# Kernel tuning notes

Hardware: AMD Instinct MI355X
Metric: run time of the kernel (lower is better)

## Reference

```python
import jax, jax.numpy as jnp
import numpy as np

B, T, TKV, D, H = 4, 2048, 512, 1024, 16
HD = D // H  # 64
HIDDEN = ((int(D * 4 * 2 / 3) + 7) // 8) * 8  # 2736
EPS = 1e-6


def setup_inputs() -> dict:
    key = jax.random.key(0)
    ks = jax.random.split(key, 16)
    x = jax.random.normal(ks[0], (B, T, D), jnp.float32)
    memory = jax.random.normal(ks[1], (B, TKV, D), jnp.float32)
    # RoPE frequencies: (T, HD//2, 2) = (cos, sin)
    inv_freq = 1.0 / (10000.0 ** (jnp.arange(0, HD, 2, dtype=jnp.float32) / HD))
    angles = jnp.arange(T, dtype=jnp.float32)[:, None] * inv_freq[None, :]
    freqs_cis = jnp.stack([jnp.cos(angles), jnp.sin(angles)], axis=-1)
    # causal mask (T, T): 0 on/below diag, -inf above
    causal_mask = jnp.where(jnp.tril(jnp.ones((T, T), bool)), 0.0, -jnp.inf).astype(jnp.float32)
    s = 0.02
    w = lambda k, i, o: jax.random.normal(k, (i, o), jnp.float32) * s  # stored as (in, out)
    return {
        'x': x, 'memory': memory, 'freqs_cis': freqs_cis, 'causal_mask': causal_mask,
        'sa_wq': w(ks[2], D, D), 'sa_wk': w(ks[3], D, D), 'sa_wv': w(ks[4], D, D), 'sa_wo': w(ks[5], D, D),
        'ca_wq': w(ks[6], D, D), 'ca_wk': w(ks[7], D, D), 'ca_wv': w(ks[8], D, D), 'ca_wo': w(ks[9], D, D),
        'w1': w(ks[10], D, HIDDEN), 'w3': w(ks[11], D, HIDDEN), 'w2': w(ks[12], HIDDEN, D),
        'g_sa': jnp.ones((D,), jnp.float32), 'g_ca': jnp.ones((D,), jnp.float32), 'g_ffn': jnp.ones((D,), jnp.float32),
    }


def rmsnorm(x, g):
    return x * jax.lax.rsqrt(jnp.mean(x * x, axis=-1, keepdims=True) + EPS) * g


def apply_rope(t, f):
    # t: (B, H, T, HD); f: (T, HD//2, 2)
    tr = t.reshape(*t.shape[:-1], HD // 2, 2)
    a, b = tr[..., 0], tr[..., 1]
    cos, sin = f[None, None, :, :, 0], f[None, None, :, :, 1]
    out = jnp.stack([a * cos - b * sin, a * sin + b * cos], axis=-1)
    return out.reshape(t.shape)


def heads(x, w):
    # (B, S, D) @ (D, D) -> (B, H, S, HD)
    b, s, _ = x.shape
    return (x @ w).reshape(b, s, H, HD).transpose(0, 2, 1, 3)


def attention(xq, kv, wq, wk, wv, wo, freqs=None, mask=None):
    q, k, v = heads(xq, wq), heads(kv, wk), heads(kv, wv)
    if freqs is not None:
        q, k = apply_rope(q, freqs), apply_rope(k, freqs)
    attn = jnp.einsum('bhqd,bhkd->bhqk', q, k) * (HD ** -0.5)
    if mask is not None:
        attn = attn + mask
    attn = jax.nn.softmax(attn, axis=-1)
    out = jnp.einsum('bhqk,bhkd->bhqd', attn, v)
    out = out.transpose(0, 2, 1, 3).reshape(xq.shape[0], xq.shape[1], D)
    return out @ wo


def reference(x, memory, freqs_cis, causal_mask,
              sa_wq, sa_wk, sa_wv, sa_wo,
              ca_wq, ca_wk, ca_wv, ca_wo,
              w1, w2, w3, g_sa, g_ca, g_ffn):
    x = rmsnorm(x + attention(x, x, sa_wq, sa_wk, sa_wv, sa_wo, freqs=freqs_cis, mask=causal_mask), g_sa)
    x = rmsnorm(x + attention(x, memory, ca_wq, ca_wk, ca_wv, ca_wo), g_ca)
    ffn = (jax.nn.silu(x @ w1) * (x @ w3)) @ w2
    x = rmsnorm(x + ffn, g_ffn)
    return x
```

## Files before the change

### kernel.cpp

```cpp
#include <hip/hip_runtime.h>
#include <hip/hip_bf16.h>

typedef __attribute__((ext_vector_type(8))) short s16x8;
typedef __attribute__((ext_vector_type(4))) float f32x4;
typedef __attribute__((ext_vector_type(16))) float f32x16;
typedef unsigned short u16;
typedef unsigned int u32;
typedef unsigned long long u64;

#define MFMA(a,b,c) __builtin_amdgcn_mfma_f32_16x16x32_bf16(a,b,c,0,0,0)
#define MFMA32(a,b,c) __builtin_amdgcn_mfma_f32_32x32x16_bf16(a,b,c,0,0,0)

constexpr int B_ = 4, T_ = 2048, TKV_ = 512, D_ = 1024, H_ = 16, HD_ = 64;
constexpr int HID_ = 2736, HIDP_ = 2816;

__device__ __forceinline__ float bf2f(u16 x) {
    union { float f; u32 u; } c; c.u = ((u32)x) << 16; return c.f;
}
__device__ __forceinline__ u16 f2bf(float f) {
    union { float f; u32 u; } c; c.f = f;
    u32 r = c.u + 0x7fffu + ((c.u >> 16) & 1u);
    return (u16)(r >> 16);
}

__device__ __forceinline__ void gload16(const void* g, void* l) {
    __builtin_amdgcn_global_load_lds(
        (const __attribute__((address_space(1))) u32*)g,
        (__attribute__((address_space(3))) u32*)l, 16, 0, 0);
}

__global__ __launch_bounds__(256) void wt_cast(const float* __restrict__ W, u16* __restrict__ WT,
                                               int K, int N, int Kp, int Np) {
    __shared__ float t[32][33];
    int tid = threadIdx.x;
    int tx = tid & 31, ty = tid >> 5;
    int n0 = blockIdx.x * 32, k0 = blockIdx.y * 32;
#pragma unroll
    for (int i = 0; i < 4; ++i) {
        int kk = k0 + ty + i * 8, nn = n0 + tx;
        t[ty + i * 8][tx] = (kk < K && nn < N) ? W[(size_t)kk * N + nn] : 0.f;
    }
    __syncthreads();
#pragma unroll
    for (int i = 0; i < 4; ++i) {
        int nn = n0 + ty + i * 8, kk = k0 + tx;
        WT[(size_t)nn * Kp + kk] = f2bf(t[tx][ty + i * 8]);
    }
}

__global__ __launch_bounds__(256) void cast_bf16(const float* __restrict__ in, u16* __restrict__ out, int n4) {
    int i = blockIdx.x * 256 + threadIdx.x;
    if (i >= n4) return;
    float4 v = ((const float4*)in)[i];
    u64 pk = (u64)f2bf(v.x) | ((u64)f2bf(v.y) << 16) | ((u64)f2bf(v.z) << 32) | ((u64)f2bf(v.w) << 48);
    ((u64*)out)[i] = pk;
}

__device__ __forceinline__ void gemm_store(void* C, const u16* mul, size_t idx, float v, int mode) {
    if (mode == 0) {
        ((float*)C)[idx] = v;
    } else if (mode == 1) {
        ((u16*)C)[idx] = f2bf(v);
    } else if (mode == 2) {
        float sg = 1.f / (1.f + __expf(-v));
        ((u16*)C)[idx] = f2bf(v * sg);
    } else if (mode == 3) {
        float h = bf2f(mul[idx]);
        ((u16*)C)[idx] = f2bf(v * h);
    } else {
        ((u16*)C)[idx] = f2bf(v * 0.125f);
    }
}


__global__ __launch_bounds__(256) void gemm_bf16(const u16* __restrict__ A, const u16* __restrict__ Bt,
                                                 void* __restrict__ C, const u16* __restrict__ mul,
                                                 int M, int N, int K, int mode, int nwg) {
    __shared__ __align__(16) u16 As[128 * 64];
    __shared__ __align__(16) u16 Bs[128 * 64];
    const int tid = threadIdx.x;
    const int lane = tid & 63, wid = tid >> 6;
    const int wr = wid >> 1, wc = wid & 1;
    const int li = lane & 15, g = lane >> 4;

    int bid = (int)blockIdx.x;
    bid = (bid & 7) * (nwg >> 3) + (bid >> 3);

    const int tn = N >> 7;
    const int m0 = (bid / tn) * 128, n0 = (bid % tn) * 128;

    const int rowst = tid >> 3;
    const int colb = (((tid & 7) ^ ((tid >> 3) & 7)) * 16);
    const char* ga = (const char*)A + ((size_t)(m0 + rowst) * K) * 2 + colb;
    const char* gb = (const char*)Bt + ((size_t)(n0 + rowst) * K) * 2 + colb;
    const size_t rstride = (size_t)32 * K * 2;

    f32x4 acc[4][4] = {};
    const int nt = K >> 6;

    for (int t = 0; t < nt; ++t) {
#pragma unroll
        for (int i = 0; i < 4; ++i) {
            gload16(ga + (size_t)t * 128 + i * rstride, (char*)As + i * 4096 + wid * 1024);
            gload16(gb + (size_t)t * 128 + i * rstride, (char*)Bs + i * 4096 + wid * 1024);
        }
        __syncthreads();
#pragma unroll
        for (int kk = 0; kk < 2; ++kk) {
            s16x8 aF[4], bF[4];
            const int sl = ((kk << 2) | g) ^ (li & 7);
#pragma unroll
            for (int m = 0; m < 4; ++m) aF[m] = *(const s16x8*)&As[(wr * 64 + m * 16 + li) * 64 + sl * 8];
#pragma unroll
            for (int n = 0; n < 4; ++n) bF[n] = *(const s16x8*)&Bs[(wc * 64 + n * 16 + li) * 64 + sl * 8];
#pragma unroll
            for (int m = 0; m < 4; ++m)
#pragma unroll
                for (int n = 0; n < 4; ++n)
                    acc[m][n] = MFMA(aF[m], bF[n], acc[m][n]);
        }
        __syncthreads();
    }

#pragma unroll
    for (int m = 0; m < 4; ++m)
#pragma unroll
        for (int n = 0; n < 4; ++n)
#pragma unroll
            for (int r = 0; r < 4; ++r) {
                size_t row = m0 + wr * 64 + m * 16 + g * 4 + r;
                size_t col = n0 + wc * 64 + n * 16 + li;
                gemm_store(C, mul, row * N + col, acc[m][n][r], mode);
            }
}

__global__ __launch_bounds__(256) void gemm_w13(const u16* __restrict__ A, const u16* __restrict__ B1t,
                                                const u16* __restrict__ B3t, u16* __restrict__ Hout,
                                                int M, int N, int K, int nwg) {
    __shared__ __align__(16) u16 As[128 * 64];
    __shared__ __align__(16) u16 B1s[128 * 64];
    __shared__ __align__(16) u16 B3s[128 * 64];
    const int tid = threadIdx.x;
    const int lane = tid & 63, wid = tid >> 6;
    const int wr = wid >> 1, wc = wid & 1;
    const int li = lane & 15, g = lane >> 4;

    int bid = (int)blockIdx.x;
    bid = (bid & 7) * (nwg >> 3) + (bid >> 3);

    const int tn = N >> 7;
    const int m0 = (bid / tn) * 128, n0 = (bid % tn) * 128;

    const int rowst = tid >> 3;
    const int colb = (((tid & 7) ^ ((tid >> 3) & 7)) * 16);
    const char* ga = (const char*)A + ((size_t)(m0 + rowst) * K) * 2 + colb;
    const char* gb1 = (const char*)B1t + ((size_t)(n0 + rowst) * K) * 2 + colb;
    const char* gb3 = (const char*)B3t + ((size_t)(n0 + rowst) * K) * 2 + colb;
    const size_t rstride = (size_t)32 * K * 2;

    f32x4 acc1[4][4] = {}, acc3[4][4] = {};
    const int nt = K >> 6;

    for (int t = 0; t < nt; ++t) {
#pragma unroll
        for (int i = 0; i < 4; ++i) {
            gload16(ga + (size_t)t * 128 + i * rstride, (char*)As + i * 4096 + wid * 1024);
            gload16(gb1 + (size_t)t * 128 + i * rstride, (char*)B1s + i * 4096 + wid * 1024);
            gload16(gb3 + (size_t)t * 128 + i * rstride, (char*)B3s + i * 4096 + wid * 1024);
        }
        __syncthreads();
#pragma unroll
        for (int kk = 0; kk < 2; ++kk) {
            const int sl = ((kk << 2) | g) ^ (li & 7);
            s16x8 aF[4];
#pragma unroll
            for (int m = 0; m < 4; ++m) aF[m] = *(const s16x8*)&As[(wr * 64 + m * 16 + li) * 64 + sl * 8];
            {
                s16x8 bF[4];
#pragma unroll
                for (int n = 0; n < 4; ++n) bF[n] = *(const s16x8*)&B1s[(wc * 64 + n * 16 + li) * 64 + sl * 8];
#pragma unroll
                for (int m = 0; m < 4; ++m)
#pragma unroll
                    for (int n = 0; n < 4; ++n)
                        acc1[m][n] = MFMA(aF[m], bF[n], acc1[m][n]);
            }
            {
                s16x8 bF[4];
#pragma unroll
                for (int n = 0; n < 4; ++n) bF[n] = *(const s16x8*)&B3s[(wc * 64 + n * 16 + li) * 64 + sl * 8];
#pragma unroll
                for (int m = 0; m < 4; ++m)
#pragma unroll
                    for (int n = 0; n < 4; ++n)
                        acc3[m][n] = MFMA(aF[m], bF[n], acc3[m][n]);
            }
        }
        __syncthreads();
    }

#pragma unroll
    for (int m = 0; m < 4; ++m)
#pragma unroll
        for (int n = 0; n < 4; ++n)
#pragma unroll
            for (int r = 0; r < 4; ++r) {
                size_t row = m0 + wr * 64 + m * 16 + g * 4 + r;
                size_t col = n0 + wc * 64 + n * 16 + li;
                float h1 = acc1[m][n][r];
                float h3 = acc3[m][n][r];
                float sg = 1.f / (1.f + __expf(-h1));
                Hout[row * N + col] = f2bf(h1 * sg * h3);
            }
}

__global__ __launch_bounds__(256) void rope_qk(u16* __restrict__ q, u16* __restrict__ k,
                                               const float* __restrict__ fr, int S) {
    size_t idx = (size_t)blockIdx.x * 256 + threadIdx.x;
    int i = (int)(idx & 31);
    int h = (int)((idx >> 5) & 15);
    size_t bt = idx >> 9;
    int t = (int)(bt & (T_ - 1));
    float2 cs = ((const float2*)fr)[t * 32 + i];
    size_t off = bt * (size_t)S + h * 64 + 2 * i;
    {
        u32* p = (u32*)(q + off);
        u32 w = *p;
        float a = bf2f((u16)(w & 0xffff)), b = bf2f((u16)(w >> 16));
        *p = (u32)f2bf((a * cs.x - b * cs.y) * 0.125f) | ((u32)f2bf((a * cs.y + b * cs.x) * 0.125f) << 16);
    }
    {
        u32* p = (u32*)(k + off);
        u32 w = *p;
        float a = bf2f((u16)(w & 0xffff)), b = bf2f((u16)(w >> 16));
        *p = (u32)f2bf(a * cs.x - b * cs.y) | ((u32)f2bf(a * cs.y + b * cs.x) << 16);
    }
}

__global__ __launch_bounds__(256) void vtrans(const u16* __restrict__ v, u16* __restrict__ vT,
                                              int Tk, int S) {
    __shared__ u16 tile[32][34];
    int bh = blockIdx.x;
    int t0 = blockIdx.y * 32, d0 = blockIdx.z * 32;
    int b = bh >> 4, h = bh & 15;
    int tid = threadIdx.x;
    int tx = tid & 31, ty = tid >> 5;
#pragma unroll
    for (int i = 0; i < 4; ++i)
        tile[ty + i * 8][tx] = v[((size_t)b * Tk + t0 + ty + i * 8) * S + h * 64 + d0 + tx];
    __syncthreads();
#pragma unroll
    for (int i = 0; i < 4; ++i)
        vT[((size_t)bh * 64 + d0 + ty + i * 8) * Tk + t0 + tx] = tile[tx][ty + i * 8];
}

__device__ __forceinline__ void attn32(const u16* __restrict__ qh, const u16* __restrict__ kh,
                                       const u16* __restrict__ vh, u16* __restrict__ oh,
                                       int q0, int nkb, int Tk, int causal, int lq, int hi,
                                       int QS, int KS) {
    const u16* qb = qh + (size_t)(q0 + lq) * QS;
    s16x8 qf[4];
#pragma unroll
    for (int c = 0; c < 4; ++c) qf[c] = *(const s16x8*)&qb[c * 16 + hi * 8];

    f32x16 o0 = {}, o1 = {};
    float mr = -1e30f, lr = 0.f;

    for (int kb = 0; kb < nkb; ++kb) {
        const int ks = kb * 32;
        f32x16 s = {};
        const u16* kp = kh + (size_t)(ks + lq) * KS + hi * 8;
#pragma unroll
        for (int c = 0; c < 4; ++c) {
            s16x8 kf = *(const s16x8*)&kp[c * 16];
            s = MFMA32(kf, qf[c], s);
        }
        if (causal && kb == nkb - 1) {
#pragma unroll
            for (int r = 0; r < 16; ++r) {
                int kl = (r & 3) + 8 * (r >> 2) + 4 * hi;
                if (kl > lq) s[r] = -1e30f;
            }
        }
        float bm = fmaxf(fmaxf(fmaxf(s[0], s[1]), fmaxf(s[2], s[3])),
                         fmaxf(fmaxf(s[4], s[5]), fmaxf(s[6], s[7])));
        float bm2 = fmaxf(fmaxf(fmaxf(s[8], s[9]), fmaxf(s[10], s[11])),
                          fmaxf(fmaxf(s[12], s[13]), fmaxf(s[14], s[15])));
        bm = fmaxf(bm, bm2);
        bm = fmaxf(bm, __shfl_xor(bm, 32));
        float mn = fmaxf(mr, bm);
        float sc = __expf(mr - mn);
        mr = mn;
        float p[16];
        float rs = 0.f;
#pragma unroll
        for (int r = 0; r < 16; ++r) { p[r] = __expf(s[r] - mn); rs += p[r]; }
        rs += __shfl_xor(rs, 32);
        lr = lr * sc + rs;
#pragma unroll
        for (int r = 0; r < 16; ++r) { o0[r] *= sc; o1[r] *= sc; }

        u32 pk[8];
#pragma unroll
        for (int i = 0; i < 8; ++i)
            pk[i] = (u32)f2bf(p[2 * i]) | ((u32)f2bf(p[2 * i + 1]) << 16);
        u32 e1 = __shfl_xor(hi ? pk[0] : pk[2], 32);
        u32 e2 = __shfl_xor(hi ? pk[1] : pk[3], 32);
        u32 e3 = __shfl_xor(hi ? pk[4] : pk[6], 32);
        u32 e4 = __shfl_xor(hi ? pk[5] : pk[7], 32);
        union { s16x8 v; u32 w[4]; } pf0, pf1;
        pf0.w[0] = hi ? e1 : pk[0];
        pf0.w[1] = hi ? e2 : pk[1];
        pf0.w[2] = hi ? pk[2] : e1;
        pf0.w[3] = hi ? pk[3] : e2;
        pf1.w[0] = hi ? e3 : pk[4];
        pf1.w[1] = hi ? e4 : pk[5];
        pf1.w[2] = hi ? pk[6] : e3;
        pf1.w[3] = hi ? pk[7] : e4;

        const u16* v0 = vh + (size_t)lq * Tk + ks + hi * 8;
        const u16* v1 = vh + (size_t)(32 + lq) * Tk + ks + hi * 8;
        o0 = MFMA32(*(const s16x8*)&v0[0],  pf0.v, o0);
        o0 = MFMA32(*(const s16x8*)&v0[16], pf1.v, o0);
        o1 = MFMA32(*(const s16x8*)&v1[0],  pf0.v, o1);
        o1 = MFMA32(*(const s16x8*)&v1[16], pf1.v, o1);
    }

    float inv = 1.f / lr;
    u16* ob = oh + (size_t)(q0 + lq) * D_;
#pragma unroll
    for (int r = 0; r < 16; ++r) {
        int hd = (r & 3) + 8 * (r >> 2) + 4 * hi;
        ob[hd] = f2bf(o0[r] * inv);
        ob[hd + 32] = f2bf(o1[r] * inv);
    }
}

__global__ __launch_bounds__(256) void attn_causal32(const u16* __restrict__ q, const u16* __restrict__ k,
                                                     const u16* __restrict__ vT, u16* __restrict__ o,
                                                     int Tq, int Tk, int QS, int KS) {
    const int lane = threadIdx.x & 63, wid = threadIdx.x >> 6;
    const int lq = lane & 31, hi = lane >> 5;
    const int ntile = Tq / 32;
    const int ppb = (ntile / 2) / 4;
    const int bh = blockIdx.x / ppb;
    const int p = (blockIdx.x % ppb) * 4 + wid;
    const int b = bh >> 4, h = bh & 15;

    const u16* qh = q + ((size_t)b * Tq) * QS + h * 64;
    const u16* kh = k + ((size_t)b * Tk) * KS + h * 64;
    const u16* vh = vT + ((size_t)bh * 64) * Tk;
    u16* oh = o + ((size_t)b * Tq) * D_ + h * 64;

    const int tA = p, tB = ntile - 1 - p;
    attn32(qh, kh, vh, oh, tA * 32, tA + 1, Tk, 1, lq, hi, QS, KS);
    attn32(qh, kh, vh, oh, tB * 32, tB + 1, Tk, 1, lq, hi, QS, KS);
}

__global__ __launch_bounds__(256) void attn_plain32(const u16* __restrict__ q, const u16* __restrict__ k,
                                                    const u16* __restrict__ vT, u16* __restrict__ o,
                                                    int Tq, int Tk, int QS, int KS) {
    const int lane = threadIdx.x & 63, wid = threadIdx.x >> 6;
    const int lq = lane & 31, hi = lane >> 5;
    const int tpb = (Tq / 32) / 4;
    const int bh = blockIdx.x / tpb;
    const int qt = (blockIdx.x % tpb) * 4 + wid;
    const int b = bh >> 4, h = bh & 15;

    const u16* qh = q + ((size_t)b * Tq) * QS + h * 64;
    const u16* kh = k + ((size_t)b * Tk) * KS + h * 64;
    const u16* vh = vT + ((size_t)bh * 64) * Tk;
    u16* oh = o + ((size_t)b * Tq) * D_ + h * 64;

    attn32(qh, kh, vh, oh, qt * 32, Tk / 32, Tk, 0, lq, hi, QS, KS);
}

__global__ __launch_bounds__(256) void addnorm(const float* __restrict__ xa, const u16* __restrict__ xb,
                                               const float* __restrict__ gg, float* __restrict__ fo,
                                               u16* __restrict__ bo) {
    int row = blockIdx.x * 4 + (threadIdx.x >> 6);
    int lane = threadIdx.x & 63;
    const float4* pa = (const float4*)(xa + (size_t)row * D_);
    const u64* pb = (const u64*)(xb + (size_t)row * D_);
    float4 v[4];
    float ss = 0.f;
#pragma unroll
    for (int j = 0; j < 4; ++j) {
        float4 a = pa[lane + 64 * j];
        u64 bw = pb[lane + 64 * j];
        v[j].x = a.x + bf2f((u16)(bw));
        v[j].y = a.y + bf2f((u16)(bw >> 16));
        v[j].z = a.z + bf2f((u16)(bw >> 32));
        v[j].w = a.w + bf2f((u16)(bw >> 48));
        ss += v[j].x * v[j].x + v[j].y * v[j].y + v[j].z * v[j].z + v[j].w * v[j].w;
    }
    ss += __shfl_xor(ss, 1);
    ss += __shfl_xor(ss, 2);
    ss += __shfl_xor(ss, 4);
    ss += __shfl_xor(ss, 8);
    ss += __shfl_xor(ss, 16);
    ss += __shfl_xor(ss, 32);
    float s = rsqrtf(ss * (1.0f / D_) + 1e-6f);
#pragma unroll
    for (int j = 0; j < 4; ++j) {
        float4 gv = ((const float4*)gg)[lane + 64 * j];
        float yx = v[j].x * s * gv.x, yy = v[j].y * s * gv.y;
        float yz = v[j].z * s * gv.z, yw = v[j].w * s * gv.w;
        if (fo) {
            float4 o4; o4.x = yx; o4.y = yy; o4.z = yz; o4.w = yw;
            ((float4*)(fo + (size_t)row * D_))[lane + 64 * j] = o4;
        }
        if (bo) {
            u64 pk = (u64)f2bf(yx) | ((u64)f2bf(yy) << 16) | ((u64)f2bf(yz) << 32) | ((u64)f2bf(yw) << 48);
            ((u64*)(bo + (size_t)row * D_))[lane + 64 * j] = pk;
        }
    }
}

extern "C" void kernel_launch(void* const* d_in, const int* in_sizes, int n_in,
                              void* d_out, int out_size, void* d_ws, size_t ws_size,
                              hipStream_t stream) {
    const float* x    = (const float*)d_in[0];
    const float* mem  = (const float*)d_in[1];
    const float* fr   = (const float*)d_in[2];
    const float* wsaq = (const float*)d_in[4];
    const float* wsak = (const float*)d_in[5];
    const float* wsav = (const float*)d_in[6];
    const float* wsao = (const float*)d_in[7];
    const float* wcaq = (const float*)d_in[8];
    const float* wcak = (const float*)d_in[9];
    const float* wcav = (const float*)d_in[10];
    const float* wcao = (const float*)d_in[11];
    const float* w1   = (const float*)d_in[12];
    const float* w3   = (const float*)d_in[13];
    const float* w2   = (const float*)d_in[14];
    const float* g_sa = (const float*)d_in[15];
    const float* g_ca = (const float*)d_in[16];
    const float* g_ff = (const float*)d_in[17];
    float* outF = (float*)d_out;

    char* p = (char*)d_ws;
    auto alloc = [&](size_t bytes) { char* r = p; p += (bytes + 255) & ~(size_t)255; return r; };
    const size_t DD2 = (size_t)1024 * 1024 * 2;
    u16* wqkvT = (u16*)alloc(3 * DD2);
    u16* saoT  = (u16*)alloc(DD2);
    u16* caqT  = (u16*)alloc(DD2);
    u16* wkvT  = (u16*)alloc(2 * DD2);
    u16* caoT  = (u16*)alloc(DD2);
    u16* w1T   = (u16*)alloc((size_t)HIDP_ * 1024 * 2);
    u16* w3T   = (u16*)alloc((size_t)HIDP_ * 1024 * 2);
    u16* w2T   = (u16*)alloc((size_t)1024 * HIDP_ * 2);
    u16* Ab    = (u16*)alloc((size_t)8192 * 1024 * 2);
    u16* memb  = (u16*)alloc((size_t)2048 * 1024 * 2);
    char* qkvRaw = alloc((size_t)8192 * 3072 * 2);
    u16* qkvb = (u16*)qkvRaw;
    u16* kvb  = (u16*)qkvRaw;
    u16* caqb = (u16*)(qkvRaw + (size_t)25165824);
    u16* vtb  = (u16*)alloc((size_t)8192 * 1024 * 2);
    u16* ob   = (u16*)alloc((size_t)8192 * 1024 * 2);
    u16* Pb   = (u16*)alloc((size_t)8192 * 1024 * 2);
    float* Rf = (float*)alloc((size_t)8192 * 1024 * 4);
    u16* Hb   = (u16*)alloc((size_t)8192 * HIDP_ * 2);

    dim3 blk(256);

    wt_cast<<<dim3(32, 32), blk, 0, stream>>>(wsaq, wqkvT,               1024, 1024, 1024, 1024);
    wt_cast<<<dim3(32, 32), blk, 0, stream>>>(wsak, wqkvT + 1024 * 1024, 1024, 1024, 1024, 1024);
    wt_cast<<<dim3(32, 32), blk, 0, stream>>>(wsav, wqkvT + 2048 * 1024, 1024, 1024, 1024, 1024);
    wt_cast<<<dim3(32, 32), blk, 0, stream>>>(wsao, saoT, 1024, 1024, 1024, 1024);
    wt_cast<<<dim3(32, 32), blk, 0, stream>>>(wcaq, caqT, 1024, 1024, 1024, 1024);
    wt_cast<<<dim3(32, 32), blk, 0, stream>>>(wcak, wkvT,               1024, 1024, 1024, 1024);
    wt_cast<<<dim3(32, 32), blk, 0, stream>>>(wcav, wkvT + 1024 * 1024, 1024, 1024, 1024, 1024);
    wt_cast<<<dim3(32, 32), blk, 0, stream>>>(wcao, caoT, 1024, 1024, 1024, 1024);
    wt_cast<<<dim3(88, 32), blk, 0, stream>>>(w1, w1T, 1024, HID_, 1024, HIDP_);
    wt_cast<<<dim3(88, 32), blk, 0, stream>>>(w3, w3T, 1024, HID_, 1024, HIDP_);
    wt_cast<<<dim3(32, 88), blk, 0, stream>>>(w2, w2T, HID_, 1024, HIDP_, 1024);

    cast_bf16<<<8192, blk, 0, stream>>>(x, Ab, 2097152);
    cast_bf16<<<2048, blk, 0, stream>>>(mem, memb, 524288);

    gemm_bf16<<<1536, blk, 0, stream>>>(Ab, wqkvT, qkvb, nullptr, 8192, 3072, 1024, 1, 1536);
    rope_qk<<<16384, blk, 0, stream>>>(qkvb, qkvb + 1024, fr, 3072);
    vtrans<<<dim3(64, 64, 2), blk, 0, stream>>>(qkvb + 2048, vtb, 2048, 3072);
    attn_causal32<<<512, blk, 0, stream>>>(qkvb, qkvb + 1024, vtb, ob, 2048, 2048, 3072, 3072);
    gemm_bf16<<<512, blk, 0, stream>>>(ob, saoT, Pb, nullptr, 8192, 1024, 1024, 1, 512);
    addnorm<<<2048, blk, 0, stream>>>(x, Pb, g_sa, Rf, Ab);

    gemm_bf16<<<512, blk, 0, stream>>>(Ab, caqT, caqb, nullptr, 8192, 1024, 1024, 4, 512);
    gemm_bf16<<<256, blk, 0, stream>>>(memb, wkvT, kvb, nullptr, 2048, 2048, 1024, 1, 256);
    vtrans<<<dim3(64, 16, 2), blk, 0, stream>>>(kvb + 1024, vtb, 512, 2048);
    attn_plain32<<<1024, blk, 0, stream>>>(caqb, kvb, vtb, ob, 2048, 512, 1024, 2048);
    gemm_bf16<<<512, blk, 0, stream>>>(ob, caoT, Pb, nullptr, 8192, 1024, 1024, 1, 512);
    addnorm<<<2048, blk, 0, stream>>>(Rf, Pb, g_ca, Rf, Ab);

    gemm_w13<<<1408, blk, 0, stream>>>(Ab, w1T, w3T, Hb, 8192, HIDP_, 1024, 1408);
    gemm_bf16<<<512, blk, 0, stream>>>(Hb, w2T, Pb, nullptr, 8192, 1024, HIDP_, 1, 512);
    addnorm<<<2048, blk, 0, stream>>>(Rf, Pb, g_ff, outF, nullptr);
}
```

Before: 801.9 us.

## Fuse paired causal query tiles into one KV loop sharing K/V loads

The causal attention kernel used to process its two balanced query tiles (p and ntile-1-p) in sequence, loading K and V twice. Both tiles now run in a single loop over KV blocks. Each K and V fragment is loaded once and feeds both tiles' MFMAs, and tile A's work is predicated off once its diagonal is passed. Global/L2 traffic for K/V and loop overhead drop, at the cost of roughly doubling the accumulator registers, which may reduce occupancy or cause spills.

```diff
diff --git a/kernel.cpp b/kernel.cpp
--- a/kernel.cpp
+++ b/kernel.cpp
@@ -254,6 +254,58 @@
         vT[((size_t)bh * 64 + d0 + ty + i * 8) * Tk + t0 + tx] = tile[tx][ty + i * 8];
 }
 
+__device__ __forceinline__ void sm_pack(const f32x16& s, int hi, float& mr, float& lr,
+                                        f32x16& o0, f32x16& o1, s16x8& pf0v, s16x8& pf1v) {
+    float bm = fmaxf(fmaxf(fmaxf(s[0], s[1]), fmaxf(s[2], s[3])),
+                     fmaxf(fmaxf(s[4], s[5]), fmaxf(s[6], s[7])));
+    float bm2 = fmaxf(fmaxf(fmaxf(s[8], s[9]), fmaxf(s[10], s[11])),
+                      fmaxf(fmaxf(s[12], s[13]), fmaxf(s[14], s[15])));
+    bm = fmaxf(bm, bm2);
+    bm = fmaxf(bm, __shfl_xor(bm, 32));
+    float mn = fmaxf(mr, bm);
+    float sc = __expf(mr - mn);
+    mr = mn;
+    float p[16];
+    float rs = 0.f;
+#pragma unroll
+    for (int r = 0; r < 16; ++r) { p[r] = __expf(s[r] - mn); rs += p[r]; }
+    rs += __shfl_xor(rs, 32);
+    lr = lr * sc + rs;
+#pragma unroll
+    for (int r = 0; r < 16; ++r) { o0[r] *= sc; o1[r] *= sc; }
+
+    u32 pk[8];
+#pragma unroll
+    for (int i = 0; i < 8; ++i)
+        pk[i] = (u32)f2bf(p[2 * i]) | ((u32)f2bf(p[2 * i + 1]) << 16);
+    u32 e1 = __shfl_xor(hi ? pk[0] : pk[2], 32);
+    u32 e2 = __shfl_xor(hi ? pk[1] : pk[3], 32);
+    u32 e3 = __shfl_xor(hi ? pk[4] : pk[6], 32);
+    u32 e4 = __shfl_xor(hi ? pk[5] : pk[7], 32);
+    union { s16x8 v; u32 w[4]; } pf0, pf1;
+    pf0.w[0] = hi ? e1 : pk[0];
+    pf0.w[1] = hi ? e2 : pk[1];
+    pf0.w[2] = hi ? pk[2] : e1;
+    pf0.w[3] = hi ? pk[3] : e2;
+    pf1.w[0] = hi ? e3 : pk[4];
+    pf1.w[1] = hi ? e4 : pk[5];
+    pf1.w[2] = hi ? pk[6] : e3;
+    pf1.w[3] = hi ? pk[7] : e4;
+    pf0v = pf0.v;
+    pf1v = pf1.v;
+}
+
+__device__ __forceinline__ void attn_out(u16* ob, const f32x16& o0, const f32x16& o1,
+                                         float lr, int hi) {
+    float inv = 1.f / lr;
+#pragma unroll
+    for (int r = 0; r < 16; ++r) {
+        int hd = (r & 3) + 8 * (r >> 2) + 4 * hi;
+        ob[hd] = f2bf(o0[r] * inv);
+        ob[hd + 32] = f2bf(o1[r] * inv);
+    }
+}
+
 __device__ __forceinline__ void attn32(const u16* __restrict__ qh, const u16* __restrict__ kh,
                                        const u16* __restrict__ vh, u16* __restrict__ oh,
                                        int q0, int nkb, int Tk, int causal, int lq, int hi,
@@ -282,63 +334,22 @@
                 if (kl > lq) s[r] = -1e30f;
             }
         }
-        float bm = fmaxf(fmaxf(fmaxf(s[0], s[1]), fmaxf(s[2], s[3])),
-                         fmaxf(fmaxf(s[4], s[5]), fmaxf(s[6], s[7])));
-        float bm2 = fmaxf(fmaxf(fmaxf(s[8], s[9]), fmaxf(s[10], s[11])),
-                          fmaxf(fmaxf(s[12], s[13]), fmaxf(s[14], s[15])));
-        bm = fmaxf(bm, bm2);
-        bm = fmaxf(bm, __shfl_xor(bm, 32));
-        float mn = fmaxf(mr, bm);
-        float sc = __expf(mr - mn);
-        mr = mn;
-        float p[16];
-        float rs = 0.f;
-#pragma unroll
-        for (int r = 0; r < 16; ++r) { p[r] = __expf(s[r] - mn); rs += p[r]; }
-        rs += __shfl_xor(rs, 32);
-        lr = lr * sc + rs;
-#pragma unroll
-        for (int r = 0; r < 16; ++r) { o0[r] *= sc; o1[r] *= sc; }
-
-        u32 pk[8];
-#pragma unroll
-        for (int i = 0; i < 8; ++i)
-            pk[i] = (u32)f2bf(p[2 * i]) | ((u32)f2bf(p[2 * i + 1]) << 16);
-        u32 e1 = __shfl_xor(hi ? pk[0] : pk[2], 32);
-        u32 e2 = __shfl_xor(hi ? pk[1] : pk[3], 32);
-        u32 e3 = __shfl_xor(hi ? pk[4] : pk[6], 32);
-        u32 e4 = __shfl_xor(hi ? pk[5] : pk[7], 32);
-        union { s16x8 v; u32 w[4]; } pf0, pf1;
-        pf0.w[0] = hi ? e1 : pk[0];
-        pf0.w[1] = hi ? e2 : pk[1];
-        pf0.w[2] = hi ? pk[2] : e1;
-        pf0.w[3] = hi ? pk[3] : e2;
-        pf1.w[0] = hi ? e3 : pk[4];
-        pf1.w[1] = hi ? e4 : pk[5];
-        pf1.w[2] = hi ? pk[6] : e3;
-        pf1.w[3] = hi ? pk[7] : e4;
+        s16x8 pf0, pf1;
+        sm_pack(s, hi, mr, lr, o0, o1, pf0, pf1);
 
         const u16* v0 = vh + (size_t)lq * Tk + ks + hi * 8;
         const u16* v1 = vh + (size_t)(32 + lq) * Tk + ks + hi * 8;
-        o0 = MFMA32(*(const s16x8*)&v0[0],  pf0.v, o0);
-        o0 = MFMA32(*(const s16x8*)&v0[16], pf1.v, o0);
-        o1 = MFMA32(*(const s16x8*)&v1[0],  pf0.v, o1);
-        o1 = MFMA32(*(const s16x8*)&v1[16], pf1.v, o1);
-    }
-
-    float inv = 1.f / lr;
-    u16* ob = oh + (size_t)(q0 + lq) * D_;
-#pragma unroll
-    for (int r = 0; r < 16; ++r) {
-        int hd = (r & 3) + 8 * (r >> 2) + 4 * hi;
-        ob[hd] = f2bf(o0[r] * inv);
-        ob[hd + 32] = f2bf(o1[r] * inv);
-    }
-}
-
-__global__ __launch_bounds__(256) void attn_causal32(const u16* __restrict__ q, const u16* __restrict__ k,
-                                                     const u16* __restrict__ vT, u16* __restrict__ o,
-                                                     int Tq, int Tk, int QS, int KS) {
+        o0 = MFMA32(*(const s16x8*)&v0[0],  pf0, o0);
+        o0 = MFMA32(*(const s16x8*)&v0[16], pf1, o0);
+        o1 = MFMA32(*(const s16x8*)&v1[0],  pf0, o1);
+        o1 = MFMA32(*(const s16x8*)&v1[16], pf1, o1);
+    }
+    attn_out(oh + (size_t)(q0 + lq) * D_, o0, o1, lr, hi);
+}
+
+__global__ __launch_bounds__(256) void attn_causal_pair(const u16* __restrict__ q, const u16* __restrict__ k,
+                                                        const u16* __restrict__ vT, u16* __restrict__ o,
+                                                        int Tq, int Tk, int QS, int KS) {
     const int lane = threadIdx.x & 63, wid = threadIdx.x >> 6;
     const int lq = lane & 31, hi = lane >> 5;
     const int ntile = Tq / 32;
@@ -353,8 +364,77 @@
     u16* oh = o + ((size_t)b * Tq) * D_ + h * 64;
 
     const int tA = p, tB = ntile - 1 - p;
-    attn32(qh, kh, vh, oh, tA * 32, tA + 1, Tk, 1, lq, hi, QS, KS);
-    attn32(qh, kh, vh, oh, tB * 32, tB + 1, Tk, 1, lq, hi, QS, KS);
+    const int q0A = tA * 32, q0B = tB * 32;
+
+    s16x8 qfA[4], qfB[4];
+    {
+        const u16* qbA = qh + (size_t)(q0A + lq) * QS;
+        const u16* qbB = qh + (size_t)(q0B + lq) * QS;
+#pragma unroll
+        for (int c = 0; c < 4; ++c) {
+            qfA[c] = *(const s16x8*)&qbA[c * 16 + hi * 8];
+            qfB[c] = *(const s16x8*)&qbB[c * 16 + hi * 8];
+        }
+    }
+
+    f32x16 oA0 = {}, oA1 = {}, oB0 = {}, oB1 = {};
+    float mrA = -1e30f, lrA = 0.f, mrB = -1e30f, lrB = 0.f;
+
+    for (int kb = 0; kb <= tB; ++kb) {
+        const int ks = kb * 32;
+        const bool doA = (kb <= tA);
+        const u16* kp = kh + (size_t)(ks + lq) * KS + hi * 8;
+        s16x8 kf[4];
+#pragma unroll
+        for (int c = 0; c < 4; ++c) kf[c] = *(const s16x8*)&kp[c * 16];
+
+        f32x16 sA = {}, sB = {};
+        if (doA) {
+#pragma unroll
+            for (int c = 0; c < 4; ++c) sA = MFMA32(kf[c], qfA[c], sA);
+        }
+#pragma unroll
+        for (int c = 0; c < 4; ++c) sB = MFMA32(kf[c], qfB[c], sB);
+
+        const u16* v0p = vh + (size_t)lq * Tk + ks + hi * 8;
+        const u16* v1p = vh + (size_t)(32 + lq) * Tk + ks + hi * 8;
+        s16x8 v00 = *(const s16x8*)&v0p[0],  v01 = *(const s16x8*)&v0p[16];
+        s16x8 v10 = *(const s16x8*)&v1p[0],  v11 = *(const s16x8*)&v1p[16];
+
+        if (doA) {
+            if (kb == tA) {
+#pragma unroll
+                for (int r = 0; r < 16; ++r) {
+                    int kl = (r & 3) + 8 * (r >> 2) + 4 * hi;
+                    if (kl > lq) sA[r] = -1e30f;
+                }
+            }
+            s16x8 pf0, pf1;
+            sm_pack(sA, hi, mrA, lrA, oA0, oA1, pf0, pf1);
+            oA0 = MFMA32(v00, pf0, oA0);
+            oA0 = MFMA32(v01, pf1, oA0);
+            oA1 = MFMA32(v10, pf0, oA1);
+            oA1 = MFMA32(v11, pf1, oA1);
+        }
+        {
+            if (kb == tB) {
+#pragma unroll
+                for (int r = 0; r < 16; ++r) {
+                    int kl = (r & 3) + 8 * (r >> 2) + 4 * hi;
+                    if (kl > lq) sB[r] = -1e30f;
+                }
+            }
+            s16x8 pf0, pf1;
+            sm_pack(sB, hi, mrB, lrB, oB0, oB1, pf0, pf1);
+            oB0 = MFMA32(v00, pf0, oB0);
+            oB0 = MFMA32(v01, pf1, oB0);
+            oB1 = MFMA32(v10, pf0, oB1);
+            oB1 = MFMA32(v11, pf1, oB1);
+        }
+    }
+
+    attn_out(oh + (size_t)(q0A + lq) * D_, oA0, oA1, lrA, hi);
+    attn_out(oh + (size_t)(q0B + lq) * D_, oB0, oB1, lrB, hi);
 }
 
 __global__ __launch_bounds__(256) void attn_plain32(const u16* __restrict__ q, const u16* __restrict__ k,
@@ -482,7 +562,7 @@
     gemm_bf16<<<1536, blk, 0, stream>>>(Ab, wqkvT, qkvb, nullptr, 8192, 3072, 1024, 1, 1536);
     rope_qk<<<16384, blk, 0, stream>>>(qkvb, qkvb + 1024, fr, 3072);
     vtrans<<<dim3(64, 64, 2), blk, 0, stream>>>(qkvb + 2048, vtb, 2048, 3072);
-    attn_causal32<<<512, blk, 0, stream>>>(qkvb, qkvb + 1024, vtb, ob, 2048, 2048, 3072, 3072);
+    attn_causal_pair<<<512, blk, 0, stream>>>(qkvb, qkvb + 1024, vtb, ob, 2048, 2048, 3072, 3072);
     gemm_bf16<<<512, blk, 0, stream>>>(ob, saoT, Pb, nullptr, 8192, 1024, 1024, 1, 512);
     addnorm<<<2048, blk, 0, stream>>>(x, Pb, g_sa, Rf, Ab);
 
```

Result: faster. 776.9 us (median of 2 runs) (-3.1%).
